# Kernel tuning notes

Hardware: AMD Instinct MI355X
Metric: run time of the kernel (lower is better)

Reference implementation:

```python
import jax, jax.numpy as jnp
import numpy as np

TAU = 1.0


def setup_inputs() -> dict:
    key = jax.random.key(0)
    k1, k2, k3 = jax.random.split(key, 3)
    B, S, V = 2, 2048, 32000
    p = jax.random.normal(k1, (B, S, V), dtype=jnp.float32)
    q = jax.random.normal(k2, (B, S, V), dtype=jnp.float32)
    mask = jax.random.randint(k3, (B, S), 0, 2).astype(bool)
    return {"p": p, "q": q, "mask": mask}


def reference(p, q, mask):
    # Faithful to the torch module: p[mask], q[mask] selects valid tokens;
    # here we keep static shapes and weight by the mask instead.
    lp = jax.nn.log_softmax(p / TAU, axis=-1)   # [B,S,V] log-probs
    lq = jax.nn.log_softmax(q / TAU, axis=-1)
    m = 0.5 * (lp + lq)                          # mean of LOG-probs (as in source)
    # KLDivLoss(log_target=True)(input=m, target=lp) = sum exp(lp) * (lp - m)
    kl_p = jnp.sum(jnp.exp(lp) * (lp - m), axis=-1)  # [B,S]
    kl_q = jnp.sum(jnp.exp(lq) * (lq - m), axis=-1)  # [B,S]
    w = mask.astype(lp.dtype)
    n = jnp.maximum(jnp.sum(w), 1.0)  # batchmean: divide by masked-token count
    return 0.5 * jnp.sum((kl_p + kl_q) * w) / n
```

## Files before the change

kernel.cpp:

```cpp
#include <hip/hip_runtime.h>
#include <math.h>

#define THREADS 256
#define PARTS   8
#define LOG2E 1.44269504088896340736f
#define LN2   0.69314718055994530942f

typedef float fx4 __attribute__((ext_vector_type(4)));

__device__ __forceinline__ void chunk_acc(
    const fx4 a0, const fx4 a1, const fx4 b0, const fx4 b1,
    float& sa, float& ta, float& sb, float& tb)
{
    float ya[8], yb[8], d[8];
    #pragma unroll
    for (int k = 0; k < 4; ++k) {
        ya[k]     = a0[k] * LOG2E;
        ya[k + 4] = a1[k] * LOG2E;
        yb[k]     = b0[k] * LOG2E;
        yb[k + 4] = b1[k] * LOG2E;
    }
    #pragma unroll
    for (int k = 0; k < 8; ++k) d[k] = ya[k] - yb[k];

    float ea[8], eb[8];
    #pragma unroll
    for (int k = 0; k < 8; ++k) { ea[k] = exp2f(ya[k]); eb[k] = exp2f(yb[k]); }

    float esa = ((ea[0] + ea[1]) + (ea[2] + ea[3])) + ((ea[4] + ea[5]) + (ea[6] + ea[7]));
    float esb = ((eb[0] + eb[1]) + (eb[2] + eb[3])) + ((eb[4] + eb[5]) + (eb[6] + eb[7]));
    float ga0 = __builtin_fmaf(ea[1], d[1], ea[0] * d[0]);
    float ga1 = __builtin_fmaf(ea[3], d[3], ea[2] * d[2]);
    float ga2 = __builtin_fmaf(ea[5], d[5], ea[4] * d[4]);
    float ga3 = __builtin_fmaf(ea[7], d[7], ea[6] * d[6]);
    float gb0 = __builtin_fmaf(eb[1], d[1], eb[0] * d[0]);
    float gb1 = __builtin_fmaf(eb[3], d[3], eb[2] * d[2]);
    float gb2 = __builtin_fmaf(eb[5], d[5], eb[4] * d[4]);
    float gb3 = __builtin_fmaf(eb[7], d[7], eb[6] * d[6]);
    sa += esa;
    sb += esb;
    ta += (ga0 + ga1) + (ga2 + ga3);
    tb += (gb0 + gb1) + (gb2 + gb3);
}

__global__ __launch_bounds__(THREADS) void jsd_rows(
    const float* __restrict__ p, const float* __restrict__ q,
    const int* __restrict__ mask, float* __restrict__ partials, int V)
{
    const int row  = blockIdx.x >> 3;
    const int part = blockIdx.x & (PARTS - 1);
    if (mask[row] == 0) return;

    const int tid = threadIdx.x;
    const size_t base = (size_t)row * (size_t)V;
    const fx4* p4 = reinterpret_cast<const fx4*>(p + base);
    const fx4* q4 = reinterpret_cast<const fx4*>(q + base);

    const int n8  = V >> 3;
    const int cpp = (n8 + PARTS - 1) / PARTS;
    const int c0  = part * cpp;
    const int c1e = min(c0 + cpp, n8);

    float sa0 = 0.f, ta0 = 0.f, sb0 = 0.f, tb0 = 0.f;
    float sa1 = 0.f, ta1 = 0.f, sb1 = 0.f, tb1 = 0.f;

    int i = c0 + tid;
    for (; i + THREADS < c1e; i += 2 * THREADS) {
        const int j = i + THREADS;
        const fx4 a0 = __builtin_nontemporal_load(p4 + 2 * i);
        const fx4 a1 = __builtin_nontemporal_load(p4 + 2 * i + 1);
        const fx4 b0 = __builtin_nontemporal_load(q4 + 2 * i);
        const fx4 b1 = __builtin_nontemporal_load(q4 + 2 * i + 1);
        const fx4 c0v = __builtin_nontemporal_load(p4 + 2 * j);
        const fx4 c1v = __builtin_nontemporal_load(p4 + 2 * j + 1);
        const fx4 d0v = __builtin_nontemporal_load(q4 + 2 * j);
        const fx4 d1v = __builtin_nontemporal_load(q4 + 2 * j + 1);
        chunk_acc(a0, a1, b0, b1, sa0, ta0, sb0, tb0);
        chunk_acc(c0v, c1v, d0v, d1v, sa1, ta1, sb1, tb1);
    }
    if (i < c1e) {
        const fx4 a0 = __builtin_nontemporal_load(p4 + 2 * i);
        const fx4 a1 = __builtin_nontemporal_load(p4 + 2 * i + 1);
        const fx4 b0 = __builtin_nontemporal_load(q4 + 2 * i);
        const fx4 b1 = __builtin_nontemporal_load(q4 + 2 * i + 1);
        chunk_acc(a0, a1, b0, b1, sa0, ta0, sb0, tb0);
    }

    float sa = sa0 + sa1, ta = ta0 + ta1, sb = sb0 + sb1, tb = tb0 + tb1;

    if (part == PARTS - 1 && (V & 7) && tid == 0) {
        for (int jj = n8 * 8; jj < V; ++jj) {
            float yA = p[base + jj] * LOG2E, yB = q[base + jj] * LOG2E, dd = yA - yB;
            float eA = exp2f(yA), eB = exp2f(yB);
            sa += eA; ta += eA * dd;
            sb += eB; tb += eB * dd;
        }
    }

    #pragma unroll
    for (int off = 1; off < 64; off <<= 1) {
        sa += __shfl_xor(sa, off, 64);
        ta += __shfl_xor(ta, off, 64);
        sb += __shfl_xor(sb, off, 64);
        tb += __shfl_xor(tb, off, 64);
    }

    __shared__ float red[THREADS / 64][4];
    const int wave = tid >> 6;
    const int lane = tid & 63;
    if (lane == 0) {
        red[wave][0] = sa; red[wave][1] = ta;
        red[wave][2] = sb; red[wave][3] = tb;
    }
    __syncthreads();
    if (tid == 0) {
        float Sa = 0.f, Ta = 0.f, Sb = 0.f, Tb = 0.f;
        #pragma unroll
        for (int w = 0; w < THREADS / 64; ++w) {
            Sa += red[w][0]; Ta += red[w][1];
            Sb += red[w][2]; Tb += red[w][3];
        }
        float* dst = partials + (size_t)blockIdx.x * 4;
        dst[0] = Sa; dst[1] = Ta; dst[2] = Sb; dst[3] = Tb;
    }
}

__global__ __launch_bounds__(1024) void jsd_final(
    const float* __restrict__ partials, const int* __restrict__ mask,
    float* __restrict__ out, int R)
{
    const int tid = threadIdx.x;
    float sum = 0.f, cnt = 0.f;
    for (int r = tid; r < R; r += 1024) {
        if (mask[r] == 0) continue;
        const float* pr = partials + (size_t)r * PARTS * 4;
        float Sa = 0.f, Ta = 0.f, Sb = 0.f, Tb = 0.f;
        #pragma unroll
        for (int w = 0; w < PARTS; ++w) {
            Sa += pr[4*w + 0]; Ta += pr[4*w + 1];
            Sb += pr[4*w + 2]; Tb += pr[4*w + 3];
        }
        sum += LN2 * (Ta / Sa - Tb / Sb);
        cnt += 1.0f;
    }
    #pragma unroll
    for (int off = 1; off < 64; off <<= 1) {
        sum += __shfl_xor(sum, off, 64);
        cnt += __shfl_xor(cnt, off, 64);
    }
    __shared__ float ssum[16], scnt[16];
    const int wave = tid >> 6;
    const int lane = tid & 63;
    if (lane == 0) { ssum[wave] = sum; scnt[wave] = cnt; }
    __syncthreads();
    if (tid == 0) {
        float S = 0.f, C = 0.f;
        #pragma unroll
        for (int w = 0; w < 16; ++w) { S += ssum[w]; C += scnt[w]; }
        out[0] = 0.25f * S / fmaxf(C, 1.0f);
    }
}

extern "C" void kernel_launch(void* const* d_in, const int* in_sizes, int n_in,
                              void* d_out, int out_size, void* d_ws, size_t ws_size,
                              hipStream_t stream) {
    const float* p    = (const float*)d_in[0];
    const float* q    = (const float*)d_in[1];
    const int*   mask = (const int*)d_in[2];
    float*       out  = (float*)d_out;

    const int BS = in_sizes[2];
    const int V  = in_sizes[0] / BS;

    float* partials = (float*)d_ws;

    jsd_rows<<<BS * PARTS, THREADS, 0, stream>>>(p, q, mask, partials, V);
    jsd_final<<<1, 1024, 0, stream>>>(partials, mask, out, BS);
}
```

Before: 103.2 us.

## Fuse final reduction into row kernel via last-block atomic counter

Merges the two kernels into a single persistent-style launch of a fixed grid that loops over row-part items, then uses an atomic counter so the last finishing block performs the final masked reduction. This removes the second kernel launch and its dependency gap. In exchange it adds a memset on the stream, an atomic plus fences per block, and a grid-stride loop with extra barriers, and the single final block still runs serially at the end.

```diff
diff --git a/kernel.cpp b/kernel.cpp
--- a/kernel.cpp
+++ b/kernel.cpp
@@ -3,6 +3,7 @@
 
 #define THREADS 256
 #define PARTS   8
+#define GRID    4096
 #define LOG2E 1.44269504088896340736f
 #define LN2   0.69314718055994530942f
 
@@ -43,121 +44,128 @@
     tb += (gb0 + gb1) + (gb2 + gb3);
 }
 
-__global__ __launch_bounds__(THREADS) void jsd_rows(
+__global__ __launch_bounds__(THREADS) void jsd_fused(
     const float* __restrict__ p, const float* __restrict__ q,
-    const int* __restrict__ mask, float* __restrict__ partials, int V)
+    const int* __restrict__ mask, unsigned* __restrict__ counter,
+    float* __restrict__ partials, float* __restrict__ out, int V, int BS)
 {
-    const int row  = blockIdx.x >> 3;
-    const int part = blockIdx.x & (PARTS - 1);
-    if (mask[row] == 0) return;
-
-    const int tid = threadIdx.x;
-    const size_t base = (size_t)row * (size_t)V;
-    const fx4* p4 = reinterpret_cast<const fx4*>(p + base);
-    const fx4* q4 = reinterpret_cast<const fx4*>(q + base);
-
+    const int tid  = threadIdx.x;
+    const int wave = tid >> 6;
+    const int lane = tid & 63;
+    const int nItems = BS * PARTS;
     const int n8  = V >> 3;
     const int cpp = (n8 + PARTS - 1) / PARTS;
-    const int c0  = part * cpp;
-    const int c1e = min(c0 + cpp, n8);
 
-    float sa0 = 0.f, ta0 = 0.f, sb0 = 0.f, tb0 = 0.f;
-    float sa1 = 0.f, ta1 = 0.f, sb1 = 0.f, tb1 = 0.f;
+    __shared__ float red[THREADS / 64][4];
+    __shared__ int   lastFlag;
+    __shared__ float ssum[THREADS / 64], scnt[THREADS / 64];
 
-    int i = c0 + tid;
-    for (; i + THREADS < c1e; i += 2 * THREADS) {
-        const int j = i + THREADS;
-        const fx4 a0 = __builtin_nontemporal_load(p4 + 2 * i);
-        const fx4 a1 = __builtin_nontemporal_load(p4 + 2 * i + 1);
-        const fx4 b0 = __builtin_nontemporal_load(q4 + 2 * i);
-        const fx4 b1 = __builtin_nontemporal_load(q4 + 2 * i + 1);
-        const fx4 c0v = __builtin_nontemporal_load(p4 + 2 * j);
-        const fx4 c1v = __builtin_nontemporal_load(p4 + 2 * j + 1);
-        const fx4 d0v = __builtin_nontemporal_load(q4 + 2 * j);
-        const fx4 d1v = __builtin_nontemporal_load(q4 + 2 * j + 1);
-        chunk_acc(a0, a1, b0, b1, sa0, ta0, sb0, tb0);
-        chunk_acc(c0v, c1v, d0v, d1v, sa1, ta1, sb1, tb1);
-    }
-    if (i < c1e) {
-        const fx4 a0 = __builtin_nontemporal_load(p4 + 2 * i);
-        const fx4 a1 = __builtin_nontemporal_load(p4 + 2 * i + 1);
-        const fx4 b0 = __builtin_nontemporal_load(q4 + 2 * i);
-        const fx4 b1 = __builtin_nontemporal_load(q4 + 2 * i + 1);
-        chunk_acc(a0, a1, b0, b1, sa0, ta0, sb0, tb0);
+    for (int it = blockIdx.x; it < nItems; it += GRID) {
+        const int row = it >> 3;
+        if (mask[row] == 0) continue;
+        const int part = it & (PARTS - 1);
+
+        const size_t base = (size_t)row * (size_t)V;
+        const fx4* p4 = reinterpret_cast<const fx4*>(p + base);
+        const fx4* q4 = reinterpret_cast<const fx4*>(q + base);
+        const int c0  = part * cpp;
+        const int c1e = min(c0 + cpp, n8);
+
+        float sa0 = 0.f, ta0 = 0.f, sb0 = 0.f, tb0 = 0.f;
+        float sa1 = 0.f, ta1 = 0.f, sb1 = 0.f, tb1 = 0.f;
+
+        int i = c0 + tid;
+        for (; i + THREADS < c1e; i += 2 * THREADS) {
+            const int j = i + THREADS;
+            const fx4 a0  = __builtin_nontemporal_load(p4 + 2 * i);
+            const fx4 a1  = __builtin_nontemporal_load(p4 + 2 * i + 1);
+            const fx4 b0  = __builtin_nontemporal_load(q4 + 2 * i);
+            const fx4 b1  = __builtin_nontemporal_load(q4 + 2 * i + 1);
+            const fx4 c0v = __builtin_nontemporal_load(p4 + 2 * j);
+            const fx4 c1v = __builtin_nontemporal_load(p4 + 2 * j + 1);
+            const fx4 d0v = __builtin_nontemporal_load(q4 + 2 * j);
+            const fx4 d1v = __builtin_nontemporal_load(q4 + 2 * j + 1);
+            chunk_acc(a0, a1, b0, b1, sa0, ta0, sb0, tb0);
+            chunk_acc(c0v, c1v, d0v, d1v, sa1, ta1, sb1, tb1);
+        }
+        if (i < c1e) {
+            const fx4 a0 = __builtin_nontemporal_load(p4 + 2 * i);
+            const fx4 a1 = __builtin_nontemporal_load(p4 + 2 * i + 1);
+            const fx4 b0 = __builtin_nontemporal_load(q4 + 2 * i);
+            const fx4 b1 = __builtin_nontemporal_load(q4 + 2 * i + 1);
+            chunk_acc(a0, a1, b0, b1, sa0, ta0, sb0, tb0);
+        }
+
+        float sa = sa0 + sa1, ta = ta0 + ta1, sb = sb0 + sb1, tb = tb0 + tb1;
+
+        if (part == PARTS - 1 && (V & 7) && tid == 0) {
+            for (int jj = n8 * 8; jj < V; ++jj) {
+                float yA = p[base + jj] * LOG2E, yB = q[base + jj] * LOG2E, dd = yA - yB;
+                float eA = exp2f(yA), eB = exp2f(yB);
+                sa += eA; ta += eA * dd;
+                sb += eB; tb += eB * dd;
+            }
+        }
+
+        #pragma unroll
+        for (int off = 1; off < 64; off <<= 1) {
+            sa += __shfl_xor(sa, off, 64);
+            ta += __shfl_xor(ta, off, 64);
+            sb += __shfl_xor(sb, off, 64);
+            tb += __shfl_xor(tb, off, 64);
+        }
+        if (lane == 0) {
+            red[wave][0] = sa; red[wave][1] = ta;
+            red[wave][2] = sb; red[wave][3] = tb;
+        }
+        __syncthreads();
+        if (tid == 0) {
+            float Sa = 0.f, Ta = 0.f, Sb = 0.f, Tb = 0.f;
+            #pragma unroll
+            for (int w = 0; w < THREADS / 64; ++w) {
+                Sa += red[w][0]; Ta += red[w][1];
+                Sb += red[w][2]; Tb += red[w][3];
+            }
+            float* dst = partials + (size_t)it * 4;
+            dst[0] = Sa; dst[1] = Ta; dst[2] = Sb; dst[3] = Tb;
+        }
+        __syncthreads();
     }
 
-    float sa = sa0 + sa1, ta = ta0 + ta1, sb = sb0 + sb1, tb = tb0 + tb1;
-
-    if (part == PARTS - 1 && (V & 7) && tid == 0) {
-        for (int jj = n8 * 8; jj < V; ++jj) {
-            float yA = p[base + jj] * LOG2E, yB = q[base + jj] * LOG2E, dd = yA - yB;
-            float eA = exp2f(yA), eB = exp2f(yB);
-            sa += eA; ta += eA * dd;
-            sb += eB; tb += eB * dd;
-        }
-    }
-
-    #pragma unroll
-    for (int off = 1; off < 64; off <<= 1) {
-        sa += __shfl_xor(sa, off, 64);
-        ta += __shfl_xor(ta, off, 64);
-        sb += __shfl_xor(sb, off, 64);
-        tb += __shfl_xor(tb, off, 64);
-    }
-
-    __shared__ float red[THREADS / 64][4];
-    const int wave = tid >> 6;
-    const int lane = tid & 63;
-    if (lane == 0) {
-        red[wave][0] = sa; red[wave][1] = ta;
-        red[wave][2] = sb; red[wave][3] = tb;
+    if (tid == 0) {
+        __threadfence();
+        unsigned old = atomicAdd(counter, 1u);
+        lastFlag = (old == (unsigned)(GRID - 1)) ? 1 : 0;
     }
     __syncthreads();
-    if (tid == 0) {
-        float Sa = 0.f, Ta = 0.f, Sb = 0.f, Tb = 0.f;
+    if (lastFlag) {
+        __threadfence();
+        float sum = 0.f, cnt = 0.f;
+        for (int r = tid; r < BS; r += THREADS) {
+            if (mask[r] == 0) continue;
+            const float* pr = partials + (size_t)r * PARTS * 4;
+            float Sa = 0.f, Ta = 0.f, Sb = 0.f, Tb = 0.f;
+            #pragma unroll
+            for (int w = 0; w < PARTS; ++w) {
+                Sa += pr[4 * w + 0]; Ta += pr[4 * w + 1];
+                Sb += pr[4 * w + 2]; Tb += pr[4 * w + 3];
+            }
+            sum += LN2 * (Ta / Sa - Tb / Sb);
+            cnt += 1.0f;
+        }
         #pragma unroll
-        for (int w = 0; w < THREADS / 64; ++w) {
-            Sa += red[w][0]; Ta += red[w][1];
-            Sb += red[w][2]; Tb += red[w][3];
+        for (int off = 1; off < 64; off <<= 1) {
+            sum += __shfl_xor(sum, off, 64);
+            cnt += __shfl_xor(cnt, off, 64);
         }
-        float* dst = partials + (size_t)blockIdx.x * 4;
-        dst[0] = Sa; dst[1] = Ta; dst[2] = Sb; dst[3] = Tb;
-    }
-}
-
-__global__ __launch_bounds__(1024) void jsd_final(
-    const float* __restrict__ partials, const int* __restrict__ mask,
-    float* __restrict__ out, int R)
-{
-    const int tid = threadIdx.x;
-    float sum = 0.f, cnt = 0.f;
-    for (int r = tid; r < R; r += 1024) {
-        if (mask[r] == 0) continue;
-        const float* pr = partials + (size_t)r * PARTS * 4;
-        float Sa = 0.f, Ta = 0.f, Sb = 0.f, Tb = 0.f;
-        #pragma unroll
-        for (int w = 0; w < PARTS; ++w) {
-            Sa += pr[4*w + 0]; Ta += pr[4*w + 1];
-            Sb += pr[4*w + 2]; Tb += pr[4*w + 3];
+        if (lane == 0) { ssum[wave] = sum; scnt[wave] = cnt; }
+        __syncthreads();
+        if (tid == 0) {
+            float S = 0.f, C = 0.f;
+            #pragma unroll
+            for (int w = 0; w < THREADS / 64; ++w) { S += ssum[w]; C += scnt[w]; }
+            out[0] = 0.25f * S / fmaxf(C, 1.0f);
         }
-        sum += LN2 * (Ta / Sa - Tb / Sb);
-        cnt += 1.0f;
-    }
-    #pragma unroll
-    for (int off = 1; off < 64; off <<= 1) {
-        sum += __shfl_xor(sum, off, 64);
-        cnt += __shfl_xor(cnt, off, 64);
-    }
-    __shared__ float ssum[16], scnt[16];
-    const int wave = tid >> 6;
-    const int lane = tid & 63;
-    if (lane == 0) { ssum[wave] = sum; scnt[wave] = cnt; }
-    __syncthreads();
-    if (tid == 0) {
-        float S = 0.f, C = 0.f;
-        #pragma unroll
-        for (int w = 0; w < 16; ++w) { S += ssum[w]; C += scnt[w]; }
-        out[0] = 0.25f * S / fmaxf(C, 1.0f);
     }
 }
 
@@ -172,8 +180,9 @@
     const int BS = in_sizes[2];
     const int V  = in_sizes[0] / BS;
 
-    float* partials = (float*)d_ws;
+    unsigned* counter  = (unsigned*)d_ws;
+    float*    partials = (float*)((char*)d_ws + 256);
 
-    jsd_rows<<<BS * PARTS, THREADS, 0, stream>>>(p, q, mask, partials, V);
-    jsd_final<<<1, 1024, 0, stream>>>(partials, mask, out, BS);
+    hipMemsetAsync(d_ws, 0, 4, stream);
+    jsd_fused<<<GRID, THREADS, 0, stream>>>(p, q, mask, counter, partials, out, V, BS);
 }
```

New measurement: 330.3 us. +220.0%, slower.
